# Optimization experiments

Measured on AMD Instinct MI355X. Metric: run time of the kernel, lower is better.

## Reference

```python
import jax, jax.numpy as jnp
import numpy as np

EMBED_DIM = 1024
NUM_HEADS = 16
HEAD_DIM = EMBED_DIM // NUM_HEADS
SCALE = float(np.sqrt(HEAD_DIM))


def setup_inputs() -> dict:
    key = jax.random.key(0)
    ks = jax.random.split(key, 5)
    B, S, D = 4, 2048, EMBED_DIM
    lim_qkv = 1.0 / np.sqrt(D)
    lim_out = 1.0 / np.sqrt(D)
    return {
        "x": jax.random.normal(ks[0], (B, S, D), dtype=jnp.float32),
        "qkv_w": jax.random.uniform(ks[1], (3 * D, D), jnp.float32, -lim_qkv, lim_qkv),
        "qkv_b": jax.random.uniform(ks[2], (3 * D,), jnp.float32, -lim_qkv, lim_qkv),
        "out_w": jax.random.uniform(ks[3], (D, D), jnp.float32, -lim_out, lim_out),
        "out_b": jax.random.uniform(ks[4], (D,), jnp.float32, -lim_out, lim_out),
    }


def reference(x, qkv_w, qkv_b, out_w, out_b):
    B, S, D = x.shape
    H, Hd = NUM_HEADS, HEAD_DIM
    # qkv projection (torch Linear: x @ W.T + b)
    qkv = x @ qkv_w.T + qkv_b                      # [B, S, 3D]
    qkv = qkv.reshape(B, S, 3, H, Hd)
    q = jnp.transpose(qkv[:, :, 0], (0, 2, 1, 3))  # [B, H, S, Hd]
    k = jnp.transpose(qkv[:, :, 1], (0, 2, 1, 3))
    v = jnp.transpose(qkv[:, :, 2], (0, 2, 1, 3))
    attn = jnp.einsum("bhqd,bhkd->bhqk", q, k) / SCALE  # [B, H, S, S]
    attn = jax.nn.softmax(attn, axis=-1)
    out = jnp.einsum("bhqk,bhkd->bhqd", attn, v)        # [B, H, S, Hd]
    out = jnp.transpose(out, (0, 2, 1, 3)).reshape(B, S, D)
    return out @ out_w.T + out_b
```

## Files before the change

kernel.cpp:

```cpp
#include <hip/hip_runtime.h>

typedef unsigned short u16;
typedef __bf16 bf16x8 __attribute__((ext_vector_type(8)));
typedef __bf16 bf16x4 __attribute__((ext_vector_type(4)));
typedef float f32x4 __attribute__((ext_vector_type(4)));
typedef float f32x16 __attribute__((ext_vector_type(16)));
typedef unsigned u32x2 __attribute__((ext_vector_type(2)));

#define AS1 __attribute__((address_space(1)))
#define AS3 __attribute__((address_space(3)))

__device__ __forceinline__ void gload_lds16(const void* g, void* l) {
  __builtin_amdgcn_global_load_lds((const AS1 void*)g, (AS3 void*)l, 16, 0, 0);
}

__device__ __forceinline__ f32x4 mfma16(bf16x8 a, bf16x8 b, f32x4 c) {
  return __builtin_amdgcn_mfma_f32_16x16x32_bf16(a, b, c, 0, 0, 0);
}
__device__ __forceinline__ f32x16 mfma32(bf16x8 a, bf16x8 b, f32x16 c) {
  return __builtin_amdgcn_mfma_f32_32x32x16_bf16(a, b, c, 0, 0, 0);
}

#define QSCALE 0.18033688011112042f

__global__ __launch_bounds__(256) void k_cvt3(const float* __restrict__ s0, u16* __restrict__ d0, int n0,
                                              const float* __restrict__ s1, u16* __restrict__ d1, int n1,
                                              const float* __restrict__ s2, u16* __restrict__ d2, int n2) {
  int g = (blockIdx.x * 256 + threadIdx.x) * 8;
  const float* src;
  u16* dst;
  int i;
  if (g < n0) { src = s0; dst = d0; i = g; }
  else if (g < n0 + n1) { src = s1; dst = d1; i = g - n0; }
  else if (g < n0 + n1 + n2) { src = s2; dst = d2; i = g - n0 - n1; }
  else return;
  float4 a = *(const float4*)(src + i);
  float4 b = *(const float4*)(src + i + 4);
  union { bf16x8 v; uint4 q; } o;
  o.v[0] = (__bf16)a.x; o.v[1] = (__bf16)a.y; o.v[2] = (__bf16)a.z; o.v[3] = (__bf16)a.w;
  o.v[4] = (__bf16)b.x; o.v[5] = (__bf16)b.y; o.v[6] = (__bf16)b.z; o.v[7] = (__bf16)b.w;
  *(uint4*)(dst + i) = o.q;
}

template <int MODE, int BXN>
__global__ __launch_bounds__(512, 2) void k_gemm_big(
    const u16* __restrict__ A, const u16* __restrict__ W,
    const float* __restrict__ bias, float* __restrict__ Cout,
    u16* __restrict__ Qo, u16* __restrict__ Ko, u16* __restrict__ Vo) {
  __shared__ __align__(16) u16 LDS[3][6 * 4096];

  const int t = threadIdx.x;
  const int lane = t & 63;
  const int w = t >> 6;
  const int wm = w >> 1;
  const int wn = w & 1;
  const int lr = lane & 15;
  const int hi = lane >> 4;

  const int TOT = BXN * 32;
  const int flat = blockIdx.x;
  const int nb = (flat & 7) * (TOT >> 3) + (flat >> 3);
  const int by = nb / BXN;
  const int bx = nb - by * BXN;
  const int m0 = by * 256;
  const int n0 = bx * 128;

  const int tt = t & 255;
  const int g = t >> 8;
  const int tu = (tt & 15) ^ (tt >> 4);
  const int sro = (tu >> 3) * 32 + (tt >> 4);
  const int scol = (tu & 7) * 8;

  auto STAGE = [&](int buf, int kt, int pLo, int pHi) {
    for (int p = pLo; p < pHi; ++p) {
      int st = p * 2 + g;
      const u16* base = (st < 4) ? (A + (size_t)(m0 + st * 64) * 1024)
                                 : (W + (size_t)(n0 + (st - 4) * 64) * 1024);
#pragma unroll
      for (int i = 0; i < 2; ++i)
        gload_lds16(base + (size_t)(sro + i * 16) * 1024 + kt * 64 + scol,
                    &LDS[buf][st * 4096 + i * 2048 + tt * 8]);
    }
  };

  f32x4 acc[4][4] = {};

  STAGE(0, 0, 0, 3);
  STAGE(1, 1, 0, 3);

  for (int kt = 0; kt < 16; ++kt) {
    const int cur = kt % 3;
    const int nxt = (kt + 2) % 3;
    if (kt < 15) asm volatile("s_waitcnt vmcnt(6)" ::: "memory");
    else         asm volatile("s_waitcnt vmcnt(0)" ::: "memory");
    __builtin_amdgcn_sched_barrier(0);
    __builtin_amdgcn_s_barrier();
    __builtin_amdgcn_sched_barrier(0);

    const u16* ab = &LDS[cur][wm * 4096];
    const u16* bb = &LDS[cur][(4 + wn) * 4096];

#pragma unroll
    for (int ks = 0; ks < 2; ++ks) {
      bf16x8 af[4], bfr[4];
#pragma unroll
      for (int mi = 0; mi < 4; ++mi)
        af[mi] = *(const bf16x8*)(ab + ((mi & 1) * 16 + lr) * 128 +
                                  (((ks * 4 + hi + 8 * (mi >> 1)) ^ lr) << 3));
#pragma unroll
      for (int ni = 0; ni < 4; ++ni)
        bfr[ni] = *(const bf16x8*)(bb + ((ni & 1) * 16 + lr) * 128 +
                                   (((ks * 4 + hi + 8 * (ni >> 1)) ^ lr) << 3));
      if (kt + 2 < 16) STAGE(nxt, kt + 2, ks ? 2 : 0, ks ? 3 : 2);
      asm volatile("s_waitcnt lgkmcnt(0)" ::: "memory");
      __builtin_amdgcn_sched_barrier(0);
      __builtin_amdgcn_s_setprio(1);
#pragma unroll
      for (int mi = 0; mi < 4; ++mi)
#pragma unroll
        for (int ni = 0; ni < 4; ++ni)
          acc[mi][ni] = mfma16(bfr[ni], af[mi], acc[mi][ni]);
      __builtin_amdgcn_s_setprio(0);
      __builtin_amdgcn_sched_barrier(0);
      if (ks == 0) __builtin_amdgcn_s_barrier();
    }
  }

  f32x4 bv[4];
#pragma unroll
  for (int ni = 0; ni < 4; ++ni)
    bv[ni] = *(const f32x4*)(bias + n0 + wn * 64 + ni * 16 + hi * 4);

  if (MODE == 0) {
    const int N = BXN * 128;
#pragma unroll
    for (int mi = 0; mi < 4; ++mi) {
      const int m = m0 + wm * 64 + mi * 16 + lr;
#pragma unroll
      for (int ni = 0; ni < 4; ++ni) {
        f32x4 o = acc[mi][ni] + bv[ni];
        *(f32x4*)(Cout + (size_t)m * N + n0 + wn * 64 + ni * 16 + hi * 4) = o;
      }
    }
  } else {
    const int bb16 = m0 >> 11;
    const int sb = (m0 & 2047) + wm * 64;
    const int which = n0 >> 10;
    const int h = ((n0 & 1023) >> 6) + wn;

    if (which < 2) {
      const float scl = (which == 0) ? QSCALE : 1.0f;
      u16* dst = ((which == 0) ? Qo : Ko) + ((size_t)(bb16 * 16 + h) * 2048) * 64;
#pragma unroll
      for (int mi = 0; mi < 4; ++mi) {
        const int s = sb + mi * 16 + lr;
#pragma unroll
        for (int ni = 0; ni < 4; ++ni) {
          bf16x4 pk;
#pragma unroll
          for (int j = 0; j < 4; ++j)
            pk[j] = (__bf16)((acc[mi][ni][j] + bv[ni][j]) * scl);
          *(bf16x4*)(dst + (size_t)s * 64 + ni * 16 + hi * 4) = pk;
        }
      }
    } else {
      __syncthreads();
      u16* scr = &LDS[0][0] + w * 4608;
#pragma unroll
      for (int mi = 0; mi < 4; ++mi)
#pragma unroll
        for (int ni = 0; ni < 4; ++ni)
#pragma unroll
          for (int j = 0; j < 4; ++j) {
            union { __bf16 b; u16 u; } cv;
            cv.b = (__bf16)(acc[mi][ni][j] + bv[ni][j]);
            scr[(ni * 16 + hi * 4 + j) * 72 + mi * 16 + lr] = cv.u;
          }
      asm volatile("s_waitcnt lgkmcnt(0)" ::: "memory");
      __builtin_amdgcn_sched_barrier(0);
      u16* dst = Vo + ((size_t)((bb16 * 16 + h) * 64 + lane)) * 2048 + sb;
#pragma unroll
      for (int mc = 0; mc < 8; ++mc) {
        bf16x8 vv = *(const bf16x8*)(scr + lane * 72 + mc * 8);
        *(bf16x8*)(dst + mc * 8) = vv;
      }
    }
  }
}

__global__ __launch_bounds__(256, 4) void k_attn(const u16* __restrict__ Q,
                                                 const u16* __restrict__ K,
                                                 const u16* __restrict__ Vt,
                                                 u16* __restrict__ ctx) {
  __shared__ __align__(16) u16 Ks[2][64 * 64];
  __shared__ __align__(16) u16 Vs[2][64 * 64];

  const int t = threadIdx.x;
  const int lane = t & 63;
  const int w = t >> 6;
  const int r31 = lane & 31;
  const int hw = lane >> 5;

  const int bid = blockIdx.x;
  const int nb = (bid & 7) * 128 + (bid >> 3);
  const int bh = nb >> 4;
  const int q0 = (nb & 15) * 128;
  const int phase = (((bid >> 8) ^ (bid >> 3)) & 3) * 8;

  const u16* qp = Q + (size_t)bh * 2048 * 64;
  const u16* kp = K + (size_t)bh * 2048 * 64;
  const u16* vp = Vt + (size_t)bh * 64 * 2048;

  const int tu = (t & 15) ^ (t >> 4);
  const int srow = (tu >> 3) * 32 + (t >> 4);
  const int scol = (tu & 7) * 8;

#pragma unroll
  for (int i = 0; i < 2; i++)
    gload_lds16(kp + (size_t)(phase * 64 + srow + i * 16) * 64 + scol,
                Ks[0] + i * 2048 + t * 8);
#pragma unroll
  for (int i = 0; i < 2; i++)
    gload_lds16(vp + (size_t)(srow + i * 16) * 2048 + phase * 64 + scol,
                Vs[0] + i * 2048 + t * 8);

  bf16x8 aq[4];
  const u16* qrow = qp + (size_t)(q0 + w * 32 + r31) * 64 + hw * 8;
#pragma unroll
  for (int kd = 0; kd < 4; kd++) aq[kd] = *(const bf16x8*)(qrow + kd * 16);

  bf16x8 ones;
#pragma unroll
  for (int e = 0; e < 8; e++) ones[e] = (__bf16)1.0f;
  const f32x16 Z = {};

  f32x16 o0 = {}, o1 = {}, l_acc = {};

  for (int it = 0; it < 32; it++) {
    const int cur = it & 1;
    asm volatile("s_waitcnt vmcnt(0)" ::: "memory");
    __builtin_amdgcn_sched_barrier(0);
    __builtin_amdgcn_s_barrier();
    __builtin_amdgcn_sched_barrier(0);

    if (it + 1 < 32) {
      const int ktn = ((it + 1 + phase) & 31) * 64;
      u16* kd_ = Ks[cur ^ 1];
      u16* vd_ = Vs[cur ^ 1];
#pragma unroll
      for (int i = 0; i < 2; i++)
        gload_lds16(kp + (size_t)(ktn + srow + i * 16) * 64 + scol,
                    kd_ + i * 2048 + t * 8);
#pragma unroll
      for (int i = 0; i < 2; i++)
        gload_lds16(vp + (size_t)(srow + i * 16) * 2048 + ktn + scol,
                    vd_ + i * 2048 + t * 8);
    }

    const u16* kb = Ks[cur];
    const u16* vb = Vs[cur];

    __builtin_amdgcn_s_setprio(1);
    f32x16 s0, s1;
    {
      bf16x8 ka0 = *(const bf16x8*)(kb + r31 * 128 + (((hw) ^ (r31 & 15)) << 3));
      bf16x8 ka1 = *(const bf16x8*)(kb + r31 * 128 + (((8 + hw) ^ (r31 & 15)) << 3));
      s0 = mfma32(ka0, aq[0], Z);
      s1 = mfma32(ka1, aq[0], Z);
    }
#pragma unroll
    for (int kd = 1; kd < 4; kd++) {
      int sl0 = (((kd * 2 + hw) ^ (r31 & 15)) << 3);
      int sl1 = (((8 + kd * 2 + hw) ^ (r31 & 15)) << 3);
      bf16x8 ka0 = *(const bf16x8*)(kb + r31 * 128 + sl0);
      bf16x8 ka1 = *(const bf16x8*)(kb + r31 * 128 + sl1);
      s0 = mfma32(ka0, aq[kd], s0);
      s1 = mfma32(ka1, aq[kd], s1);
    }
    __builtin_amdgcn_s_setprio(0);

#pragma unroll
    for (int e = 0; e < 16; e++) {
      s0[e] = __builtin_amdgcn_exp2f(s0[e]);
      s1[e] = __builtin_amdgcn_exp2f(s1[e]);
    }

    __builtin_amdgcn_s_setprio(1);
#pragma unroll
    for (int tile = 0; tile < 2; tile++) {
      f32x16 st = tile ? s1 : s0;
      unsigned pk[8];
#pragma unroll
      for (int p = 0; p < 8; p++) {
        union { __bf16 h[2]; unsigned u; } cv;
        cv.h[0] = (__bf16)st[2 * p];
        cv.h[1] = (__bf16)st[2 * p + 1];
        pk[p] = cv.u;
      }
#pragma unroll
      for (int c = 0; c < 2; c++) {
        u32x2 ra = __builtin_amdgcn_permlane32_swap(pk[4 * c], pk[4 * c + 2], false, false);
        u32x2 rb = __builtin_amdgcn_permlane32_swap(pk[4 * c + 1], pk[4 * c + 3], false, false);
        union { unsigned u[4]; bf16x8 v; } pf;
        pf.u[0] = ra[0]; pf.u[1] = rb[0]; pf.u[2] = ra[1]; pf.u[3] = rb[1];
        const int kap = tile * 2 + c;
        int slv0 = (((kap * 2 + hw) ^ (r31 & 15)) << 3);
        int slv1 = (((8 + kap * 2 + hw) ^ (r31 & 15)) << 3);
        bf16x8 v0 = *(const bf16x8*)(vb + r31 * 128 + slv0);
        bf16x8 v1 = *(const bf16x8*)(vb + r31 * 128 + slv1);
        o0 = mfma32(v0, pf.v, o0);
        o1 = mfma32(v1, pf.v, o1);
        l_acc = mfma32(ones, pf.v, l_acc);
      }
    }
    __builtin_amdgcn_s_setprio(0);
  }

  const int bb = bh >> 4, h = bh & 15;
  const float inv = 1.0f / l_acc[0];
  const size_t base = (size_t)(bb * 2048 + q0 + w * 32 + r31) * 1024 + h * 64;
#pragma unroll
  for (int g = 0; g < 4; g++) {
    bf16x4 p0, p1;
#pragma unroll
    for (int j = 0; j < 4; j++) {
      p0[j] = (__bf16)(o0[g * 4 + j] * inv);
      p1[j] = (__bf16)(o1[g * 4 + j] * inv);
    }
    *(bf16x4*)(ctx + base + g * 8 + hw * 4) = p0;
    *(bf16x4*)(ctx + base + 32 + g * 8 + hw * 4) = p1;
  }
}

extern "C" void kernel_launch(void* const* d_in, const int* in_sizes, int n_in,
                              void* d_out, int out_size, void* d_ws, size_t ws_size,
                              hipStream_t stream) {
  const float* x = (const float*)d_in[0];
  const float* qkv_w = (const float*)d_in[1];
  const float* qkv_b = (const float*)d_in[2];
  const float* out_w = (const float*)d_in[3];
  const float* out_b = (const float*)d_in[4];
  float* out = (float*)d_out;
  char* ws = (char*)d_ws;

  u16* xb    = (u16*)(ws + 0);
  u16* wqkvb = (u16*)(ws + 16777216);
  u16* wob   = (u16*)(ws + 23068672);
  u16* Qb    = (u16*)(ws + 25165824);
  u16* Kb    = (u16*)(ws + 41943040);
  u16* Vtb   = (u16*)(ws + 58720256);
  u16* ctx   = xb;

  k_cvt3<<<6144, 256, 0, stream>>>(x, xb, 8388608,
                                   qkv_w, wqkvb, 3145728,
                                   out_w, wob, 1048576);

  k_gemm_big<1, 24><<<768, 512, 0, stream>>>(xb, wqkvb, qkv_b, nullptr,
                                             Qb, Kb, Vtb);
  k_attn<<<1024, 256, 0, stream>>>(Qb, Kb, Vtb, ctx);
  k_gemm_big<0, 8><<<256, 512, 0, stream>>>(ctx, wob, out_b, out,
                                            nullptr, nullptr, nullptr);
}
```

Before: 195.6 us.

## Use dedicated 256x256-tile QKV GEMM kernel with double-buffered swizzled LDS

Splits the templated GEMM into a dedicated QKV projection kernel with 256x256 output tiles (8 waves as 2x4, each owning 128x64), 64-wide K steps and double-buffered XOR-swizzled LDS staging that is interleaved with the MFMA sub-steps. The larger tile raises arithmetic intensity and halves the grid to 384 blocks, cutting global and L2 traffic for A and W. The V transpose epilogue now runs in two halves through the LDS scratch. The costs are higher register pressure from 128 accumulator floats per lane, a single wave of blocks on the GPU, and 128 KB of LDS per block, which may limit occupancy.

Measured after the change: 197.5 us. No clear change (+1.0%).

```diff
diff --git a/kernel.cpp b/kernel.cpp
--- a/kernel.cpp
+++ b/kernel.cpp
@@ -42,11 +42,156 @@
   *(uint4*)(dst + i) = o.q;
 }
 
-template <int MODE, int BXN>
-__global__ __launch_bounds__(512, 2) void k_gemm_big(
+__global__ __launch_bounds__(512, 2) void k_qkv(
     const u16* __restrict__ A, const u16* __restrict__ W,
-    const float* __restrict__ bias, float* __restrict__ Cout,
+    const float* __restrict__ bias,
     u16* __restrict__ Qo, u16* __restrict__ Ko, u16* __restrict__ Vo) {
+  __shared__ __align__(16) u16 LDS[2][4][8192];
+
+  const int t = threadIdx.x;
+  const int lane = t & 63;
+  const int w = t >> 6;
+  const int wm2 = w >> 2;
+  const int wn4 = w & 3;
+  const int lr = lane & 15;
+  const int hi = lane >> 4;
+
+  const int flat = blockIdx.x;
+  const int nb = (flat & 7) * 48 + (flat >> 3);
+  const int by = nb / 12;
+  const int bx = nb - by * 12;
+  const int m0 = by * 256;
+  const int n0 = bx * 256;
+
+  const int tt = t & 255;
+  const int sub = t >> 8;
+  const int tu = (tt & 15) ^ (tt >> 4);
+  const int sro = (tu >> 3) * 32 + (tt >> 4);
+  const int scol = (tu & 7) * 8;
+
+  auto STAGEH = [&](int buf, int half, int kt) {
+    const u16* base = (half < 2) ? (A + (size_t)(m0 + half * 128) * 1024)
+                                 : (W + (size_t)(n0 + (half - 2) * 128) * 1024);
+#pragma unroll
+    for (int i = 0; i < 2; ++i)
+      gload_lds16(base + (size_t)(sub * 64 + sro + i * 16) * 1024 + kt * 64 + scol,
+                  &LDS[buf][half][sub * 4096 + i * 2048 + tt * 8]);
+  };
+
+  f32x4 acc[8][4] = {};
+
+  STAGEH(0, 0, 0); STAGEH(0, 1, 0); STAGEH(0, 2, 0); STAGEH(0, 3, 0);
+
+  for (int kt = 0; kt < 16; ++kt) {
+    const int cur = kt & 1;
+    asm volatile("s_waitcnt vmcnt(0)" ::: "memory");
+    __builtin_amdgcn_sched_barrier(0);
+    __builtin_amdgcn_s_barrier();
+    __builtin_amdgcn_sched_barrier(0);
+
+    const u16* ah = &LDS[cur][wm2][0];
+    const u16* bh = &LDS[cur][2 + (wn4 >> 1)][0];
+
+    bf16x8 bfr[4][2];
+#pragma unroll
+    for (int q = 0; q < 4; ++q) {
+      bf16x8 af[2][2];
+#pragma unroll
+      for (int m2 = 0; m2 < 2; ++m2) {
+        const int mi = q * 2 + m2;
+#pragma unroll
+        for (int ks = 0; ks < 2; ++ks)
+          af[m2][ks] = *(const bf16x8*)(ah + (mi >> 2) * 4096 +
+                        ((mi & 1) * 16 + lr) * 128 +
+                        ((((ks * 4 + hi) + 8 * ((mi >> 1) & 1)) ^ lr) << 3));
+      }
+      if (q == 0) {
+#pragma unroll
+        for (int ni = 0; ni < 4; ++ni)
+#pragma unroll
+          for (int ks = 0; ks < 2; ++ks)
+            bfr[ni][ks] = *(const bf16x8*)(bh + (wn4 & 1) * 4096 +
+                          ((ni & 1) * 16 + lr) * 128 +
+                          ((((ks * 4 + hi) + 8 * (ni >> 1)) ^ lr) << 3));
+      }
+      if (kt + 1 < 16) STAGEH(cur ^ 1, q, kt + 1);
+      asm volatile("s_waitcnt lgkmcnt(0)" ::: "memory");
+      __builtin_amdgcn_sched_barrier(0);
+      __builtin_amdgcn_s_setprio(1);
+#pragma unroll
+      for (int m2 = 0; m2 < 2; ++m2)
+#pragma unroll
+        for (int ni = 0; ni < 4; ++ni)
+#pragma unroll
+          for (int ks = 0; ks < 2; ++ks)
+            acc[q * 2 + m2][ni] = mfma16(bfr[ni][ks], af[m2][ks], acc[q * 2 + m2][ni]);
+      __builtin_amdgcn_s_setprio(0);
+      __builtin_amdgcn_sched_barrier(0);
+      if (q < 3) __builtin_amdgcn_s_barrier();
+    }
+  }
+
+  const int bb16 = m0 >> 11;
+  const int sb = (m0 & 2047) + wm2 * 128;
+  const int nbase = n0 + wn4 * 64;
+  const int which = nbase >> 10;
+  const int h = (nbase & 1023) >> 6;
+
+  f32x4 bv[4];
+#pragma unroll
+  for (int ni = 0; ni < 4; ++ni)
+    bv[ni] = *(const f32x4*)(bias + nbase + ni * 16 + hi * 4);
+
+  if (which < 2) {
+    const float scl = (which == 0) ? QSCALE : 1.0f;
+    u16* dst = ((which == 0) ? Qo : Ko) + ((size_t)(bb16 * 16 + h) * 2048) * 64;
+#pragma unroll
+    for (int mi = 0; mi < 8; ++mi) {
+      const int s = sb + mi * 16 + lr;
+#pragma unroll
+      for (int ni = 0; ni < 4; ++ni) {
+        bf16x4 pk;
+#pragma unroll
+        for (int j = 0; j < 4; ++j)
+          pk[j] = (__bf16)((acc[mi][ni][j] + bv[ni][j]) * scl);
+        *(bf16x4*)(dst + (size_t)s * 64 + ni * 16 + hi * 4) = pk;
+      }
+    }
+  } else {
+    __syncthreads();
+    u16* scr = &LDS[0][0][0] + w * 4608;
+#pragma unroll
+    for (int mig = 0; mig < 2; ++mig) {
+#pragma unroll
+      for (int m2 = 0; m2 < 4; ++m2) {
+        const int mi = mig * 4 + m2;
+#pragma unroll
+        for (int ni = 0; ni < 4; ++ni)
+#pragma unroll
+          for (int j = 0; j < 4; ++j) {
+            union { __bf16 b; u16 u; } cv;
+            cv.b = (__bf16)(acc[mi][ni][j] + bv[ni][j]);
+            scr[(ni * 16 + hi * 4 + j) * 72 + m2 * 16 + lr] = cv.u;
+          }
+      }
+      asm volatile("s_waitcnt lgkmcnt(0)" ::: "memory");
+      __builtin_amdgcn_sched_barrier(0);
+      u16* dst = Vo + ((size_t)((bb16 * 16 + h) * 64 + lane)) * 2048 + sb + mig * 64;
+#pragma unroll
+      for (int mc = 0; mc < 8; ++mc) {
+        bf16x8 vv = *(const bf16x8*)(scr + lane * 72 + mc * 8);
+        *(bf16x8*)(dst + mc * 8) = vv;
+      }
+      asm volatile("s_waitcnt lgkmcnt(0)" ::: "memory");
+      __builtin_amdgcn_sched_barrier(0);
+    }
+  }
+}
+
+template <int BXN>
+__global__ __launch_bounds__(512, 2) void k_gemm_out(
+    const u16* __restrict__ A, const u16* __restrict__ W,
+    const float* __restrict__ bias, float* __restrict__ Cout) {
   __shared__ __align__(16) u16 LDS[3][6 * 4096];
 
   const int t = threadIdx.x;
@@ -131,59 +276,14 @@
   for (int ni = 0; ni < 4; ++ni)
     bv[ni] = *(const f32x4*)(bias + n0 + wn * 64 + ni * 16 + hi * 4);
 
-  if (MODE == 0) {
-    const int N = BXN * 128;
-#pragma unroll
-    for (int mi = 0; mi < 4; ++mi) {
-      const int m = m0 + wm * 64 + mi * 16 + lr;
-#pragma unroll
-      for (int ni = 0; ni < 4; ++ni) {
-        f32x4 o = acc[mi][ni] + bv[ni];
-        *(f32x4*)(Cout + (size_t)m * N + n0 + wn * 64 + ni * 16 + hi * 4) = o;
-      }
-    }
-  } else {
-    const int bb16 = m0 >> 11;
-    const int sb = (m0 & 2047) + wm * 64;
-    const int which = n0 >> 10;
-    const int h = ((n0 & 1023) >> 6) + wn;
-
-    if (which < 2) {
-      const float scl = (which == 0) ? QSCALE : 1.0f;
-      u16* dst = ((which == 0) ? Qo : Ko) + ((size_t)(bb16 * 16 + h) * 2048) * 64;
-#pragma unroll
-      for (int mi = 0; mi < 4; ++mi) {
-        const int s = sb + mi * 16 + lr;
-#pragma unroll
-        for (int ni = 0; ni < 4; ++ni) {
-          bf16x4 pk;
-#pragma unroll
-          for (int j = 0; j < 4; ++j)
-            pk[j] = (__bf16)((acc[mi][ni][j] + bv[ni][j]) * scl);
-          *(bf16x4*)(dst + (size_t)s * 64 + ni * 16 + hi * 4) = pk;
-        }
-      }
-    } else {
-      __syncthreads();
-      u16* scr = &LDS[0][0] + w * 4608;
-#pragma unroll
-      for (int mi = 0; mi < 4; ++mi)
-#pragma unroll
-        for (int ni = 0; ni < 4; ++ni)
-#pragma unroll
-          for (int j = 0; j < 4; ++j) {
-            union { __bf16 b; u16 u; } cv;
-            cv.b = (__bf16)(acc[mi][ni][j] + bv[ni][j]);
-            scr[(ni * 16 + hi * 4 + j) * 72 + mi * 16 + lr] = cv.u;
-          }
-      asm volatile("s_waitcnt lgkmcnt(0)" ::: "memory");
-      __builtin_amdgcn_sched_barrier(0);
-      u16* dst = Vo + ((size_t)((bb16 * 16 + h) * 64 + lane)) * 2048 + sb;
-#pragma unroll
-      for (int mc = 0; mc < 8; ++mc) {
-        bf16x8 vv = *(const bf16x8*)(scr + lane * 72 + mc * 8);
-        *(bf16x8*)(dst + mc * 8) = vv;
-      }
+  const int N = BXN * 128;
+#pragma unroll
+  for (int mi = 0; mi < 4; ++mi) {
+    const int m = m0 + wm * 64 + mi * 16 + lr;
+#pragma unroll
+    for (int ni = 0; ni < 4; ++ni) {
+      f32x4 o = acc[mi][ni] + bv[ni];
+      *(f32x4*)(Cout + (size_t)m * N + n0 + wn * 64 + ni * 16 + hi * 4) = o;
     }
   }
 }
@@ -355,9 +455,7 @@
                                    qkv_w, wqkvb, 3145728,
                                    out_w, wob, 1048576);
 
-  k_gemm_big<1, 24><<<768, 512, 0, stream>>>(xb, wqkvb, qkv_b, nullptr,
-                                             Qb, Kb, Vtb);
+  k_qkv<<<384, 512, 0, stream>>>(xb, wqkvb, qkv_b, Qb, Kb, Vtb);
   k_attn<<<1024, 256, 0, stream>>>(Qb, Kb, Vtb, ctx);
-  k_gemm_big<0, 8><<<256, 512, 0, stream>>>(ctx, wob, out_b, out,
-                                            nullptr, nullptr, nullptr);
-}
+  k_gemm_out<8><<<256, 512, 0, stream>>>(ctx, wob, out_b, out);
+}
```
